# Kernel tuning notes

Measured on AMD Instinct MI355X. Metric: run time of the kernel, lower is better.

## Reference

```python
import jax, jax.numpy as jnp
import numpy as np

D_MODEL = 1024

def setup_inputs() -> dict:
    key = jax.random.key(0)
    ks = jax.random.split(key, 9)
    s = 1.0 / np.sqrt(D_MODEL)
    x = jax.random.normal(ks[0], (4, 2048, D_MODEL), dtype=jnp.float32)
    Wq = jax.random.uniform(ks[1], (D_MODEL, D_MODEL), jnp.float32, -s, s)
    bq = jax.random.uniform(ks[2], (D_MODEL,), jnp.float32, -s, s)
    Wk = jax.random.uniform(ks[3], (D_MODEL, D_MODEL), jnp.float32, -s, s)
    bk = jax.random.uniform(ks[4], (D_MODEL,), jnp.float32, -s, s)
    Wv = jax.random.uniform(ks[5], (D_MODEL, D_MODEL), jnp.float32, -s, s)
    bv = jax.random.uniform(ks[6], (D_MODEL,), jnp.float32, -s, s)
    Wo = jax.random.uniform(ks[7], (D_MODEL, D_MODEL), jnp.float32, -s, s)
    bo = jax.random.uniform(ks[8], (D_MODEL,), jnp.float32, -s, s)
    return {"x": x, "Wq": Wq, "bq": bq, "Wk": Wk, "bk": bk,
            "Wv": Wv, "bv": bv, "Wo": Wo, "bo": bo}

def reference(x, Wq, bq, Wk, bk, Wv, bv, Wo, bo):
    # Linear projections (weights stored as [in, out])
    q = x @ Wq + bq  # [b, s, d]
    k = x @ Wk + bk
    v = x @ Wv + bv
    d_k = q.shape[-1]
    scores = jnp.einsum("bqd,bkd->bqk", q, k) / jnp.sqrt(jnp.float32(d_k))
    p = jax.nn.softmax(scores, axis=-1)
    attn = jnp.einsum("bqk,bkd->bqd", p, v)
    return attn @ Wo + bo
```

## Files before the change

kernel.cpp:

```cpp
#include <hip/hip_runtime.h>
#include <stdint.h>

#define D_MODEL 1024
#define SEQ 2048
#define NBATCH 4

typedef __attribute__((ext_vector_type(4))) float f32x4;
typedef __attribute__((ext_vector_type(8))) __bf16 bf16x8;
typedef __attribute__((ext_vector_type(4))) unsigned short u16x4;

__device__ __forceinline__ float b2f(unsigned short u) {
    union { unsigned int i; float f; } c; c.i = ((unsigned int)u) << 16; return c.f;
}
__device__ __forceinline__ unsigned short f2b(float f) {
    union { float f; unsigned int i; } c; c.f = f;
    unsigned int u = c.i;
    u += 0x7FFFu + ((u >> 16) & 1u);
    return (unsigned short)(u >> 16);
}

__device__ __forceinline__ void glds16(void* lds, const void* g) {
    __builtin_amdgcn_global_load_lds((const __attribute__((address_space(1))) void*)g,
                                     (__attribute__((address_space(3))) void*)lds,
                                     16, 0, 0);
}

__device__ __forceinline__ void cfence() { asm volatile("" ::: "memory"); }

__device__ __forceinline__ void xcd_map(int& xx, int& yy, int& zz)
{
    const int gx = gridDim.x, gy = gridDim.y;
    int bid = blockIdx.x + gx * (blockIdx.y + gy * blockIdx.z);
    const int H = gy >> 3;
    const int xcd = bid & 7;
    int slot = bid >> 3;
    yy = xcd * H + (slot % H);
    slot /= H;
    xx = slot % gx;
    zz = slot / gx;
}

__device__ __forceinline__ void gemm_tile(const unsigned short* __restrict__ A,
                                          const unsigned short* __restrict__ Bt,
                                          int K, int m0, int n0,
                                          f32x4 (&acc)[4][4])
{
    __shared__ alignas(16) unsigned short As[3 * 256 * 32];
    __shared__ alignas(16) unsigned short Bs[3 * 128 * 32];

    const int t    = threadIdx.x;
    const int wave = t >> 6;
    const int lane = t & 63;

    const int srow = (wave << 4) + (lane >> 2);
    const int sch  = ((lane & 3) ^ ((srow >> 1) & 3)) * 8;

    const unsigned short* Ag = A  + (long)(m0 + srow) * K + sch;
    const unsigned short* Bg = Bt + (long)(n0 + srow) * K + sch;

    char* AsW = (char*)As + wave * 1024;
    char* BsW = (char*)Bs + wave * 1024;

    const int fr = lane & 15, quad = lane >> 4;
    const int wr = wave >> 1, wc = wave & 1;
    const int slot = (quad ^ ((fr >> 1) & 3)) * 16;
    const int aoff = (wr * 64 + fr) * 64 + slot;
    const int boff = (wc * 64 + fr) * 64 + slot;

    const int nt = K >> 5;

    auto stage = [&](int buf, int ko) {
        glds16(AsW + buf * 16384,        Ag + ko);
        glds16(AsW + buf * 16384 + 8192, Ag + (long)128 * K + ko);
        glds16(BsW + buf * 8192,         Bg + ko);
    };

    stage(0, 0);
    stage(1, 32);
    asm volatile("s_waitcnt vmcnt(3)" ::: "memory");
    __builtin_amdgcn_sched_barrier(0);
    cfence(); __builtin_amdgcn_s_barrier(); cfence();

    int br = 0, bw = 2, ko = 64;
    for (int ti = 0; ti < nt; ++ti) {
        const char* Ab = (const char*)As + br * 16384;
        const char* Bb = (const char*)Bs + br * 8192;
        bf16x8 af[4], bv[4];
        #pragma unroll
        for (int i = 0; i < 4; ++i)
            af[i] = *(const bf16x8*)(Ab + aoff + i * 1024);
        #pragma unroll
        for (int i = 0; i < 4; ++i)
            bv[i] = *(const bf16x8*)(Bb + boff + i * 1024);

        const bool pf = (ti + 2 < nt);
        if (pf) { stage(bw, ko); ko += 32; }

        __builtin_amdgcn_s_setprio(1);
        #pragma unroll
        for (int mi = 0; mi < 4; ++mi)
            #pragma unroll
            for (int ni = 0; ni < 4; ++ni)
                acc[mi][ni] = __builtin_amdgcn_mfma_f32_16x16x32_bf16(
                                  af[mi], bv[ni], acc[mi][ni], 0, 0, 0);
        __builtin_amdgcn_s_setprio(0);

        if (pf)               asm volatile("s_waitcnt vmcnt(3)" ::: "memory");
        else if (ti + 1 < nt) asm volatile("s_waitcnt vmcnt(0)" ::: "memory");
        __builtin_amdgcn_sched_barrier(0);
        cfence(); __builtin_amdgcn_s_barrier(); cfence();

        br = (br == 2) ? 0 : br + 1;
        bw = (bw == 2) ? 0 : bw + 1;
    }
}

template<bool BIAS, typename OutT>
__global__ __launch_bounds__(512)
void gemm_bt(const unsigned short* __restrict__ A,
             const unsigned short* __restrict__ Bt,
             const float* __restrict__ bias,
             OutT* __restrict__ C,
             int N, int K, long sA, long sB, long sC)
{
    int xx, yy, zz;
    xcd_map(xx, yy, zz);
    A  += (long)zz * sA;
    Bt += (long)zz * sB;
    C  += (long)zz * sC;
    const int m0 = yy * 256;
    const int n0 = xx * 128;

    f32x4 acc[4][4] = {};
    gemm_tile(A, Bt, K, m0, n0, acc);

    const int t = threadIdx.x, wave = t >> 6, lane = t & 63;
    const int wr = wave >> 1, wc = wave & 1;
    const int fr = lane & 15, quad = lane >> 4;

    float bb[4] = {0.f, 0.f, 0.f, 0.f};
    if (BIAS) {
        #pragma unroll
        for (int ni = 0; ni < 4; ++ni)
            bb[ni] = bias[n0 + wc * 64 + ni * 16 + fr];
    }

    #pragma unroll
    for (int mi = 0; mi < 4; ++mi) {
        const int rowb = m0 + wr * 64 + mi * 16 + quad * 4;
        #pragma unroll
        for (int ni = 0; ni < 4; ++ni) {
            const int col = n0 + wc * 64 + ni * 16 + fr;
            f32x4 v = acc[mi][ni];
            if constexpr (sizeof(OutT) == 4) {
                #pragma unroll
                for (int r = 0; r < 4; ++r)
                    C[(long)(rowb + r) * N + col] = v[r] + bb[ni];
            } else {
                #pragma unroll
                for (int r = 0; r < 4; ++r)
                    C[(long)(rowb + r) * N + col] = (OutT)f2b(v[r] + bb[ni]);
            }
        }
    }
}

__global__ __launch_bounds__(512)
void qkv_gemm(const unsigned short* __restrict__ xb,
              const unsigned short* __restrict__ Wqt,
              const unsigned short* __restrict__ Wkt,
              const unsigned short* __restrict__ Wvt,
              const float* __restrict__ bq, const float* __restrict__ bk,
              const float* __restrict__ bv,
              unsigned short* __restrict__ Q, unsigned short* __restrict__ Kb,
              unsigned short* __restrict__ Vt)
{
    int xx, yy, zz;
    xcd_map(xx, yy, zz);

    const unsigned short* Bt; const float* bias; unsigned short* C; bool tstore = false;
    switch (zz) {
        case 0:  Bt = Wqt; bias = bq; C = Q;  break;
        case 1:  Bt = Wkt; bias = bk; C = Kb; break;
        default: Bt = Wvt; bias = bv; C = Vt; tstore = true; break;
    }
    const int m0 = yy * 256;
    const int n0 = xx * 128;
    const int N = D_MODEL, K = D_MODEL;

    f32x4 acc[4][4] = {};
    gemm_tile(xb, Bt, K, m0, n0, acc);

    const int t = threadIdx.x, wave = t >> 6, lane = t & 63;
    const int wr = wave >> 1, wc = wave & 1;
    const int fr = lane & 15, quad = lane >> 4;

    float bb[4];
    #pragma unroll
    for (int ni = 0; ni < 4; ++ni)
        bb[ni] = bias[n0 + wc * 64 + ni * 16 + fr];

    #pragma unroll
    for (int mi = 0; mi < 4; ++mi) {
        const int rowb = m0 + wr * 64 + mi * 16 + quad * 4;
        #pragma unroll
        for (int ni = 0; ni < 4; ++ni) {
            const int col = n0 + wc * 64 + ni * 16 + fr;
            f32x4 v = acc[mi][ni];
            if (!tstore) {
                #pragma unroll
                for (int r = 0; r < 4; ++r)
                    C[(long)(rowb + r) * N + col] = f2b(v[r] + bb[ni]);
            } else {
                u16x4 pk;
                #pragma unroll
                for (int r = 0; r < 4; ++r)
                    pk[r] = f2b(v[r] + bb[ni]);
                unsigned short* dst = C + ((long)(rowb >> 11)) * ((long)N * SEQ)
                                        + (long)col * SEQ + (rowb & (SEQ - 1));
                *(u16x4*)dst = pk;
            }
        }
    }
}

__global__ __launch_bounds__(256)
void softmax_inplace(unsigned short* __restrict__ S)
{
    const long row = blockIdx.x;
    unsigned short* s = S + row * SEQ;
    const int t = threadIdx.x;

    u16x4 a = ((const u16x4*)s)[t];
    u16x4 b = ((const u16x4*)s)[t + 256];
    float v[8];
    #pragma unroll
    for (int i = 0; i < 4; ++i) { v[i] = b2f(a[i]); v[4 + i] = b2f(b[i]); }

    float mx = v[0];
    #pragma unroll
    for (int i = 1; i < 8; ++i) mx = fmaxf(mx, v[i]);
    #pragma unroll
    for (int off = 32; off; off >>= 1) mx = fmaxf(mx, __shfl_xor(mx, off));

    __shared__ float red[8];
    const int wv = t >> 6, ln = t & 63;
    if (ln == 0) red[wv] = mx;
    __syncthreads();
    mx = fmaxf(fmaxf(red[0], red[1]), fmaxf(red[2], red[3]));

    const float sc = 0.03125f;
    float e[8], sum = 0.f;
    #pragma unroll
    for (int i = 0; i < 8; ++i) { e[i] = __expf((v[i] - mx) * sc); sum += e[i]; }
    #pragma unroll
    for (int off = 32; off; off >>= 1) sum += __shfl_xor(sum, off);
    if (ln == 0) red[4 + wv] = sum;
    __syncthreads();
    sum = (red[4] + red[5]) + (red[6] + red[7]);
    const float inv = 1.f / sum;

    u16x4 o;
    #pragma unroll
    for (int i = 0; i < 4; ++i) o[i] = f2b(e[i] * inv);
    ((u16x4*)s)[t] = o;
    #pragma unroll
    for (int i = 0; i < 4; ++i) o[i] = f2b(e[4 + i] * inv);
    ((u16x4*)s)[t + 256] = o;
}

__global__ __launch_bounds__(256)
void prep(const float* __restrict__ x, unsigned short* __restrict__ xb,
          const float* __restrict__ W0, const float* __restrict__ W1,
          const float* __restrict__ W2, const float* __restrict__ W3,
          unsigned short* __restrict__ T0, unsigned short* __restrict__ T1,
          unsigned short* __restrict__ T2, unsigned short* __restrict__ T3)
{
    const int bid = blockIdx.x;
    if (bid < 8192) {
        long i = ((long)bid * 256 + threadIdx.x) * 4;
        f32x4 v = *(const f32x4*)(x + i);
        u16x4 o;
        #pragma unroll
        for (int r = 0; r < 4; ++r) o[r] = f2b(v[r]);
        *(u16x4*)(xb + i) = o;
        return;
    }
    const int b2 = bid - 8192;
    const float* W; unsigned short* T;
    switch (b2 >> 10) {
        case 0:  W = W0; T = T0; break;
        case 1:  W = W1; T = T1; break;
        case 2:  W = W2; T = T2; break;
        default: W = W3; T = T3; break;
    }
    const int tile = b2 & 1023;
    const int bx = (tile & 31) * 32, by = (tile >> 5) * 32;
    __shared__ float buf[32][33];
    const int tx = threadIdx.x & 31, ty = threadIdx.x >> 5;
    #pragma unroll
    for (int i = 0; i < 32; i += 8)
        buf[ty + i][tx] = W[(long)(by + ty + i) * D_MODEL + bx + tx];
    __syncthreads();
    #pragma unroll
    for (int i = 0; i < 32; i += 8)
        T[(long)(bx + ty + i) * D_MODEL + by + tx] = f2b(buf[tx][ty + i]);
}

extern "C" void kernel_launch(void* const* d_in, const int* in_sizes, int n_in,
                              void* d_out, int out_size, void* d_ws, size_t ws_size,
                              hipStream_t stream)
{
    const float* x  = (const float*)d_in[0];
    const float* Wq = (const float*)d_in[1];
    const float* bq = (const float*)d_in[2];
    const float* Wk = (const float*)d_in[3];
    const float* bk = (const float*)d_in[4];
    const float* Wv = (const float*)d_in[5];
    const float* bv = (const float*)d_in[6];
    const float* Wo = (const float*)d_in[7];
    const float* bo = (const float*)d_in[8];
    float* out = (float*)d_out;

    char* ws = (char*)d_ws;
    const size_t MB = 1024ull * 1024ull;
    unsigned short* Wqt = (unsigned short*)(ws + 0 * MB);
    unsigned short* Wkt = (unsigned short*)(ws + 2 * MB);
    unsigned short* Wvt = (unsigned short*)(ws + 4 * MB);
    unsigned short* Wot = (unsigned short*)(ws + 6 * MB);
    unsigned short* xb  = (unsigned short*)(ws + 8 * MB);
    unsigned short* Q   = (unsigned short*)(ws + 24 * MB);
    unsigned short* Kb  = (unsigned short*)(ws + 40 * MB);
    unsigned short* Vt  = (unsigned short*)(ws + 56 * MB);
    unsigned short* At  = (unsigned short*)(ws + 72 * MB);
    unsigned short* S   = (unsigned short*)(ws + 88 * MB);

    const dim3 blk256(256);
    const dim3 blk512(512);

    prep<<<dim3(12288), blk256, 0, stream>>>(x, xb, Wq, Wk, Wv, Wo, Wqt, Wkt, Wvt, Wot);

    qkv_gemm<<<dim3(8, 32, 3), blk512, 0, stream>>>(xb, Wqt, Wkt, Wvt, bq, bk, bv, Q, Kb, Vt);

    gemm_bt<false, unsigned short><<<dim3(16, 8, 4), blk512, 0, stream>>>(
        Q, Kb, nullptr, S, 2048, 1024,
        (long)2048 * 1024, (long)2048 * 1024, (long)2048 * 2048);

    softmax_inplace<<<dim3(NBATCH * SEQ), blk256, 0, stream>>>(S);

    gemm_bt<false, unsigned short><<<dim3(8, 8, 4), blk512, 0, stream>>>(
        S, Vt, nullptr, At, 1024, 2048,
        (long)2048 * 2048, (long)1024 * 2048, (long)2048 * 1024);

    gemm_bt<true, float><<<dim3(8, 32, 1), blk512, 0, stream>>>(
        At, Wot, bo, out, 1024, 1024, 0, 0, 0);
}
```

Baseline: 278.2 us.

## Restructure GEMM mainloop to 64-wide K tiles with split-phase staging

Replaces the 32-wide K, triple-buffered GEMM core with a 64-wide K tile loop. A uses three rotating buffers and B two, and each iteration issues staged async global-to-LDS loads between four MFMA phases separated by barriers. It also changes the LDS swizzle to an 8-chunk XOR pattern and raises launch bounds to request two blocks per CU. The aim is fewer barriers per K element and better overlap of memory traffic with MFMA work, at the cost of more LDS (160KB shared) and more barriers inside each iteration. That LDS footprint may stop two blocks from actually fitting on a CU.

```diff
diff --git a/kernel.cpp b/kernel.cpp
--- a/kernel.cpp
+++ b/kernel.cpp
@@ -26,6 +26,16 @@
 }
 
 __device__ __forceinline__ void cfence() { asm volatile("" ::: "memory"); }
+
+#define BAR()   do { cfence(); __builtin_amdgcn_s_barrier(); cfence(); } while (0)
+#define LGKM0() do { asm volatile("s_waitcnt lgkmcnt(0)" ::: "memory"); \
+                     __builtin_amdgcn_sched_barrier(0); } while (0)
+#define VM6()   do { asm volatile("s_waitcnt vmcnt(6)" ::: "memory"); \
+                     __builtin_amdgcn_sched_barrier(0); } while (0)
+#define VM0()   do { asm volatile("s_waitcnt vmcnt(0)" ::: "memory"); \
+                     __builtin_amdgcn_sched_barrier(0); } while (0)
+#define PRIO1   __builtin_amdgcn_s_setprio(1)
+#define PRIO0   __builtin_amdgcn_s_setprio(0)
 
 __device__ __forceinline__ void xcd_map(int& xx, int& yy, int& zz)
 {
@@ -40,83 +50,122 @@
     zz = slot / gx;
 }
 
-__device__ __forceinline__ void gemm_tile(const unsigned short* __restrict__ A,
+__device__ __forceinline__ void gemm_core(const unsigned short* __restrict__ A,
                                           const unsigned short* __restrict__ Bt,
                                           int K, int m0, int n0,
                                           f32x4 (&acc)[4][4])
 {
-    __shared__ alignas(16) unsigned short As[3 * 256 * 32];
-    __shared__ alignas(16) unsigned short Bs[3 * 128 * 32];
-
-    const int t    = threadIdx.x;
-    const int wave = t >> 6;
-    const int lane = t & 63;
-
-    const int srow = (wave << 4) + (lane >> 2);
-    const int sch  = ((lane & 3) ^ ((srow >> 1) & 3)) * 8;
-
+    __shared__ alignas(16) unsigned short AsR[3 * 256 * 64];
+    __shared__ alignas(16) unsigned short BsR[2 * 128 * 64];
+
+    const int t = threadIdx.x, w = t >> 6, l = t & 63;
+
+    const int srow = (w << 3) + (l >> 3);
+    const int sch  = ((l & 7) ^ ((l >> 3) & 7)) * 8;
     const unsigned short* Ag = A  + (long)(m0 + srow) * K + sch;
     const unsigned short* Bg = Bt + (long)(n0 + srow) * K + sch;
-
-    char* AsW = (char*)As + wave * 1024;
-    char* BsW = (char*)Bs + wave * 1024;
-
-    const int fr = lane & 15, quad = lane >> 4;
-    const int wr = wave >> 1, wc = wave & 1;
-    const int slot = (quad ^ ((fr >> 1) & 3)) * 16;
-    const int aoff = (wr * 64 + fr) * 64 + slot;
-    const int boff = (wc * 64 + fr) * 64 + slot;
-
-    const int nt = K >> 5;
-
-    auto stage = [&](int buf, int ko) {
-        glds16(AsW + buf * 16384,        Ag + ko);
-        glds16(AsW + buf * 16384 + 8192, Ag + (long)128 * K + ko);
-        glds16(BsW + buf * 8192,         Bg + ko);
+    const int woff = w * 1024;
+
+    const int fr = l & 15, quad = l >> 4;
+    const int wr = w >> 1, wc = w & 1;
+    const int sl0 = ((quad)     ^ (fr & 7)) * 16;
+    const int sl1 = ((4 + quad) ^ (fr & 7)) * 16;
+    const int aro = wr * 8192 + fr * 128;
+    const int bro = wc * 8192 + fr * 128;
+
+    char* aE = (char*)AsR;
+    char* aO = (char*)AsR + 32768;
+    char* aN = (char*)AsR + 65536;
+    char* const b0 = (char*)BsR;
+    char* const b1 = (char*)BsR + 16384;
+
+    const int nIt = K >> 7;
+
+    auto stageA = [&](char* ab, int kt) {
+        char* L = ab + woff;
+        const unsigned short* g = Ag + (long)kt * 64;
+        glds16(L,         g);
+        glds16(L +  8192, g + (long)64  * K);
+        glds16(L + 16384, g + (long)128 * K);
+        glds16(L + 24576, g + (long)192 * K);
     };
-
-    stage(0, 0);
-    stage(1, 32);
-    asm volatile("s_waitcnt vmcnt(3)" ::: "memory");
-    __builtin_amdgcn_sched_barrier(0);
-    cfence(); __builtin_amdgcn_s_barrier(); cfence();
-
-    int br = 0, bw = 2, ko = 64;
-    for (int ti = 0; ti < nt; ++ti) {
-        const char* Ab = (const char*)As + br * 16384;
-        const char* Bb = (const char*)Bs + br * 8192;
-        bf16x8 af[4], bv[4];
-        #pragma unroll
-        for (int i = 0; i < 4; ++i)
-            af[i] = *(const bf16x8*)(Ab + aoff + i * 1024);
-        #pragma unroll
-        for (int i = 0; i < 4; ++i)
-            bv[i] = *(const bf16x8*)(Bb + boff + i * 1024);
-
-        const bool pf = (ti + 2 < nt);
-        if (pf) { stage(bw, ko); ko += 32; }
-
-        __builtin_amdgcn_s_setprio(1);
-        #pragma unroll
-        for (int mi = 0; mi < 4; ++mi)
+    auto stageB = [&](char* bb, int kt) {
+        char* L = bb + woff;
+        const unsigned short* g = Bg + (long)kt * 64;
+        glds16(L,        g);
+        glds16(L + 8192, g + (long)64 * K);
+    };
+
+    bf16x8 bfr[4][2], afr[2][2];
+
+    auto loadB = [&](const char* bb) {
+        #pragma unroll
+        for (int ni = 0; ni < 4; ++ni) {
+            bfr[ni][0] = *(const bf16x8*)(bb + bro + ni * 2048 + sl0);
+            bfr[ni][1] = *(const bf16x8*)(bb + bro + ni * 2048 + sl1);
+        }
+    };
+    auto loadA = [&](const char* ab, int mlo) {
+        #pragma unroll
+        for (int j = 0; j < 2; ++j) {
+            afr[j][0] = *(const bf16x8*)(ab + aro + (mlo + j) * 2048 + sl0);
+            afr[j][1] = *(const bf16x8*)(ab + aro + (mlo + j) * 2048 + sl1);
+        }
+    };
+    auto mfma16 = [&](int mlo) {
+        #pragma unroll
+        for (int j = 0; j < 2; ++j)
             #pragma unroll
             for (int ni = 0; ni < 4; ++ni)
-                acc[mi][ni] = __builtin_amdgcn_mfma_f32_16x16x32_bf16(
-                                  af[mi], bv[ni], acc[mi][ni], 0, 0, 0);
-        __builtin_amdgcn_s_setprio(0);
-
-        if (pf)               asm volatile("s_waitcnt vmcnt(3)" ::: "memory");
-        else if (ti + 1 < nt) asm volatile("s_waitcnt vmcnt(0)" ::: "memory");
-        __builtin_amdgcn_sched_barrier(0);
-        cfence(); __builtin_amdgcn_s_barrier(); cfence();
-
-        br = (br == 2) ? 0 : br + 1;
-        bw = (bw == 2) ? 0 : bw + 1;
+                #pragma unroll
+                for (int ks = 0; ks < 2; ++ks)
+                    acc[mlo + j][ni] = __builtin_amdgcn_mfma_f32_16x16x32_bf16(
+                        afr[j][ks], bfr[ni][ks], acc[mlo + j][ni], 0, 0, 0);
+    };
+
+    stageA(aE, 0);
+    stageB(b0, 0);
+    stageA(aO, 1);
+    stageB(b1, 1);
+    VM6();
+    BAR();
+
+    for (int it = 0; it < nIt; ++it) {
+        const bool more = (it + 1 < nIt);
+        const int tE2 = 2 * it + 2;
+
+        loadB(b0); loadA(aE, 0);
+        if (more) stageA(aN, tE2);
+        BAR(); LGKM0();
+        PRIO1; mfma16(0); PRIO0;
+        BAR();
+
+        loadA(aE, 2);
+        if (more) stageB(b0, tE2);
+        BAR(); LGKM0();
+        PRIO1; mfma16(2); PRIO0;
+        if (more) { VM6(); } else { VM0(); }
+        BAR();
+
+        loadB(b1); loadA(aO, 0);
+        if (more) stageA(aE, tE2 + 1);
+        BAR(); LGKM0();
+        PRIO1; mfma16(0); PRIO0;
+        BAR();
+
+        loadA(aO, 2);
+        if (more) stageB(b1, tE2 + 1);
+        BAR(); LGKM0();
+        PRIO1; mfma16(2); PRIO0;
+        if (more) VM6();
+        BAR();
+
+        char* tmp = aN; aN = aO; aO = aE; aE = tmp;
     }
 }
 
 template<bool BIAS, typename OutT>
-__global__ __launch_bounds__(512)
+__global__ __launch_bounds__(512, 2)
 void gemm_bt(const unsigned short* __restrict__ A,
              const unsigned short* __restrict__ Bt,
              const float* __restrict__ bias,
@@ -132,7 +181,7 @@
     const int n0 = xx * 128;
 
     f32x4 acc[4][4] = {};
-    gemm_tile(A, Bt, K, m0, n0, acc);
+    gemm_core(A, Bt, K, m0, n0, acc);
 
     const int t = threadIdx.x, wave = t >> 6, lane = t & 63;
     const int wr = wave >> 1, wc = wave & 1;
@@ -165,7 +214,7 @@
     }
 }
 
-__global__ __launch_bounds__(512)
+__global__ __launch_bounds__(512, 2)
 void qkv_gemm(const unsigned short* __restrict__ xb,
               const unsigned short* __restrict__ Wqt,
               const unsigned short* __restrict__ Wkt,
@@ -189,7 +238,7 @@
     const int N = D_MODEL, K = D_MODEL;
 
     f32x4 acc[4][4] = {};
-    gemm_tile(xb, Bt, K, m0, n0, acc);
+    gemm_core(xb, Bt, K, m0, n0, acc);
 
     const int t = threadIdx.x, wave = t >> 6, lane = t & 63;
     const int wr = wave >> 1, wc = wave & 1;
```

After: 274.1 us. Within noise of the previous version (-1.5%).
